# Optimization experiments

Hardware: AMD Instinct MI355X
Metric: run time of the kernel (lower is better)

Reference implementation:

```python
import jax, jax.numpy as jnp
import numpy as np

H, DK, DV = 16, 64, 64

def setup_inputs() -> dict:
    key = jax.random.key(0)
    ks = jax.random.split(key, 5)
    S, E = 2048, 1024
    return {
        "x": jax.random.normal(ks[0], (S, E), jnp.float32),
        "Wq": jax.random.normal(ks[1], (H * DK, E), jnp.float32) * 0.02,
        "Wk": jax.random.normal(ks[2], (H * DK, E), jnp.float32) * 0.02,
        "Wv": jax.random.normal(ks[3], (H * DV, E), jnp.float32) * 0.02,
        "Wo": jax.random.normal(ks[4], (H * DV, H * DV), jnp.float32) * 0.02,
    }

def reference(x, Wq, Wk, Wv, Wo):
    S = x.shape[0]
    # Fused QKV projections (equivalent to per-head Linear with concatenated weights)
    Q = (x @ Wq.T).reshape(S, H, DK).transpose(1, 0, 2)  # [H,S,dk]
    K = (x @ Wk.T).reshape(S, H, DK).transpose(1, 0, 2)  # [H,S,dk]
    V = (x @ Wv.T).reshape(S, H, DV).transpose(1, 0, 2)  # [H,S,dv]
    scale = 1.0 / np.sqrt(DK).astype(np.float32)
    scores = jnp.einsum('hsd,htd->hst', Q, K) * scale    # [H,S,S]
    weights = jax.nn.softmax(scores, axis=-1)
    A = jnp.einsum('hst,htv->hsv', weights, V)           # [H,S,dv]
    A1 = A.transpose(1, 0, 2).reshape(S, H * DV)         # concat heads on last dim
    return A1 @ Wo.T
```

## Files before the change

kernel.cpp:

```cpp
#include <hip/hip_runtime.h>
#include <hip/hip_bf16.h>
#include <stdint.h>

typedef uint16_t u16;
typedef uint32_t u32;
typedef float    f32x4  __attribute__((ext_vector_type(4)));
typedef __bf16   bf16x8 __attribute__((ext_vector_type(8)));
typedef uint16_t u16x8  __attribute__((ext_vector_type(8)));
typedef uint16_t u16x4  __attribute__((ext_vector_type(4)));
typedef uint32_t u32x4  __attribute__((ext_vector_type(4)));

#define HH 16
#define SS 2048
#define EE 1024
#define DD 64

__device__ inline u16 f2bf(float f) {
  uint32_t u = __builtin_bit_cast(uint32_t, f);
  u += 0x7fff + ((u >> 16) & 1);
  return (u16)(u >> 16);
}
__device__ inline float bf2f(u16 b) {
  return __builtin_bit_cast(float, (uint32_t)b << 16);
}

__device__ inline u32 cvtpk(float lo, float hi) {
  u32 r;
  asm("v_cvt_pk_bf16_f32 %0, %1, %2" : "=v"(r) : "v"(lo), "v"(hi));
  return r;
}

__device__ inline void gload_lds16(const void* g, void* l) {
  __builtin_amdgcn_global_load_lds(
      (const __attribute__((address_space(1))) uint32_t*)g,
      (__attribute__((address_space(3))) uint32_t*)l, 16, 0, 0);
}

__global__ __launch_bounds__(256) void convert_kernel(
    const float* __restrict__ x,  const float* __restrict__ wq,
    const float* __restrict__ wk, const float* __restrict__ wv,
    const float* __restrict__ wo,
    u16* __restrict__ xb, u16* __restrict__ wqkvb, u16* __restrict__ wob) {
  const int64_t M1 = 1024 * 1024;
  int64_t e = ((int64_t)blockIdx.x * 256 + threadIdx.x) * 4;
  const float* src; u16* dst; int64_t off;
  if (e < 2 * M1)      { src = x;  dst = xb;           off = e; }
  else if (e < 3 * M1) { src = wq; dst = wqkvb;        off = e - 2 * M1; }
  else if (e < 4 * M1) { src = wk; dst = wqkvb + M1;   off = e - 3 * M1; }
  else if (e < 5 * M1) { src = wv; dst = wqkvb + 2*M1; off = e - 4 * M1; }
  else                 { src = wo; dst = wob;          off = e - 5 * M1; }
  float4 v = *(const float4*)(src + off);
  u16x4 o;
  o[0] = f2bf(v.x); o[1] = f2bf(v.y); o[2] = f2bf(v.z); o[3] = f2bf(v.w);
  *(u16x4*)(dst + off) = o;
}

template <int EPI, int K, int N, int BN>
__global__ __launch_bounds__(256, 4) void gemm_kernel(
    const u16* __restrict__ A, const u16* __restrict__ B,
    u16* __restrict__ q_ws, u16* __restrict__ k_ws, u16* __restrict__ vt_ws,
    float* __restrict__ Cout) {
  constexpr int BM = 64, BK = 64;
  constexpr int NFB = BN / 32;
  constexpr float C2 = 0.18033688f;
  __shared__ __align__(16) u16 As[BM * BK];
  __shared__ __align__(16) u16 Bs[BN * BK];
  const int t = threadIdx.x;
  const int lane = t & 63, w = t >> 6;
  const int wr = w >> 1, wc = w & 1;
  const int fr = lane & 15, fg = lane >> 4;

  const int nwg = gridDim.x * gridDim.y;
  const int bid = blockIdx.y * gridDim.x + blockIdx.x;
  const int swz = (bid & 7) * (nwg >> 3) + (bid >> 3);
  const int m0 = (swz / gridDim.x) * BM, n0 = (swz % gridDim.x) * BN;

  f32x4 acc[2][NFB] = {};

  for (int k0 = 0; k0 < K; k0 += BK) {
#pragma unroll
    for (int it = 0; it < 2; ++it) {
      const int c = t + it * 256, row = c >> 3, sch = (c & 7) ^ (row & 7);
      gload_lds16(A + (int64_t)(m0 + row) * K + k0 + sch * 8,
                  As + (c & ~63) * 8);
    }
#pragma unroll
    for (int it = 0; it < BN * 8 / 256; ++it) {
      const int c = t + it * 256, row = c >> 3, sch = (c & 7) ^ (row & 7);
      gload_lds16(B + (int64_t)(n0 + row) * K + k0 + sch * 8,
                  Bs + (c & ~63) * 8);
    }
    __syncthreads();
    bf16x8 af[2][2], bfr[NFB][2];
#pragma unroll
    for (int mi = 0; mi < 2; ++mi)
#pragma unroll
      for (int kc = 0; kc < 2; ++kc) {
        const int row = wr * 32 + mi * 16 + fr;
        const int cc = (kc * 4 + fg) ^ (row & 7);
        af[mi][kc] = __builtin_bit_cast(bf16x8, *(const u16x8*)&As[row * 64 + cc * 8]);
      }
#pragma unroll
    for (int ni = 0; ni < NFB; ++ni)
#pragma unroll
      for (int kc = 0; kc < 2; ++kc) {
        const int row = wc * (BN / 2) + ni * 16 + fr;
        const int cc = (kc * 4 + fg) ^ (row & 7);
        bfr[ni][kc] = __builtin_bit_cast(bf16x8, *(const u16x8*)&Bs[row * 64 + cc * 8]);
      }
#pragma unroll
    for (int kc = 0; kc < 2; ++kc)
#pragma unroll
      for (int mi = 0; mi < 2; ++mi)
#pragma unroll
        for (int ni = 0; ni < NFB; ++ni)
          acc[mi][ni] = __builtin_amdgcn_mfma_f32_16x16x32_bf16(
              af[mi][kc], bfr[ni][kc], acc[mi][ni], 0, 0, 0);
    __syncthreads();
  }

#pragma unroll
  for (int mi = 0; mi < 2; ++mi)
#pragma unroll
    for (int ni = 0; ni < NFB; ++ni)
#pragma unroll
      for (int r = 0; r < 4; ++r) {
        const int m = m0 + wr * 32 + mi * 16 + fg * 4 + r;
        const int n = n0 + wc * (BN / 2) + ni * 16 + fr;
        const float v = acc[mi][ni][r];
        if constexpr (EPI == 0) {
          const int which = n >> 10, nn = n & 1023, h = nn >> 6, d = nn & 63;
          if (which == 0)
            q_ws[((int64_t)h * SS + m) * DD + d] = f2bf(v * C2);
          else if (which == 1)
            k_ws[((int64_t)h * SS + m) * DD + d] = f2bf(v);
          else
            vt_ws[((int64_t)h * DD + d) * SS + m] = f2bf(v);
        } else {
          Cout[(int64_t)m * N + n] = v;
        }
      }
}

__global__ __launch_bounds__(256, 5) void attn_kernel(
    const u16* __restrict__ q_ws, const u16* __restrict__ k_ws,
    const u16* __restrict__ vt_ws, u16* __restrict__ opart,
    float* __restrict__ lsum) {
  constexpr int NTS = SS / 64 / 2;
  __shared__ __align__(16) u16 lds[16384];
  const int t = threadIdx.x;
  const int lane = t & 63, w = t >> 6;
  const int ql = lane & 15, g = lane >> 4;
  const int h = blockIdx.y, qb = blockIdx.x, sp = blockIdx.z;
  const int kt0 = sp * NTS;
  const int qbase = qb * 64 + w * 16;

  const u16* Qh = q_ws + ((int64_t)h * SS + qbase) * DD;
  const u16* Kh = k_ws + ((int64_t)h * SS + kt0 * 64) * DD;
  const u16* Vh = vt_ws + (int64_t)h * DD * SS + kt0 * 64;

  const int r0 = t >> 3, ch = t & 7, r1 = (t + 256) >> 3;
  const int sch0 = ch ^ (r0 & 7), sch1 = ch ^ (r1 & 7);
  const int64_t ko0 = (int64_t)r0 * DD + sch0 * 8;
  const int64_t ko1 = (int64_t)r1 * DD + sch1 * 8;
  const int64_t vo0 = (int64_t)r0 * SS + sch0 * 8;
  const int64_t vo1 = (int64_t)r1 * SS + sch1 * 8;
  const int dst0 = (t & ~63) * 8, dst1 = dst0 + 2048;

  bf16x8 qf[2];
#pragma unroll
  for (int dd = 0; dd < 2; ++dd)
    qf[dd] = __builtin_bit_cast(
        bf16x8, *(const u16x8*)(Qh + ql * DD + dd * 32 + g * 8));

  u16x8 ov;
#pragma unroll
  for (int j = 0; j < 8; ++j) ov[j] = 0x3F80;
  const bf16x8 onesf = __builtin_bit_cast(bf16x8, ov);

  f32x4 o[4] = {};
  f32x4 o_l = {};

  auto qk = [&](f32x4 (&s)[4], const int kb_) {
    __builtin_amdgcn_s_setprio(1);
#pragma unroll
    for (int kb = 0; kb < 4; ++kb) {
      const int key = kb * 16 + ql;
      f32x4 z = {};
#pragma unroll
      for (int dd = 0; dd < 2; ++dd) {
        bf16x8 kf = __builtin_bit_cast(
            bf16x8,
            *(const u16x8*)&lds[kb_ * 4096 + key * 64 +
                                (((dd * 4 + g) ^ (ql & 7)) * 8)]);
        z = __builtin_amdgcn_mfma_f32_16x16x32_bf16(kf, qf[dd], z, 0, 0, 0);
      }
      s[kb] = z;
    }
    __builtin_amdgcn_s_setprio(0);
  };

  auto smpv = [&](f32x4 (&s)[4], const int vb_) {
#pragma unroll
    for (int kb = 0; kb < 4; ++kb)
#pragma unroll
      for (int r = 0; r < 4; ++r)
        s[kb][r] = exp2f(s[kb][r]);
#pragma unroll
    for (int ks = 0; ks < 2; ++ks) {
      u32 x0 = cvtpk(s[2 * ks][0], s[2 * ks][1]);
      u32 x1 = cvtpk(s[2 * ks][2], s[2 * ks][3]);
      u32 y0 = cvtpk(s[2 * ks + 1][0], s[2 * ks + 1][1]);
      u32 y1 = cvtpk(s[2 * ks + 1][2], s[2 * ks + 1][3]);
      asm("v_permlane32_swap_b32 %0, %1" : "+v"(x0), "+v"(y0));
      asm("v_permlane16_swap_b32 %0, %1" : "+v"(x0), "+v"(y0));
      asm("v_permlane32_swap_b32 %0, %1" : "+v"(x1), "+v"(y1));
      asm("v_permlane16_swap_b32 %0, %1" : "+v"(x1), "+v"(y1));
      u32x4 aw; aw[0] = x0; aw[1] = x1; aw[2] = y0; aw[3] = y1;
      const bf16x8 pa = __builtin_bit_cast(bf16x8, aw);
      __builtin_amdgcn_s_setprio(1);
      o_l = __builtin_amdgcn_mfma_f32_16x16x32_bf16(pa, onesf, o_l, 0, 0, 0);
#pragma unroll
      for (int nb = 0; nb < 4; ++nb) {
        const int dv = nb * 16 + ql;
        bf16x8 vf = __builtin_bit_cast(
            bf16x8,
            *(const u16x8*)&lds[8192 + vb_ * 4096 + dv * 64 +
                                (((ks * 4 + g) ^ (ql & 7)) * 8)]);
        o[nb] = __builtin_amdgcn_mfma_f32_16x16x32_bf16(pa, vf, o[nb], 0, 0, 0);
      }
      __builtin_amdgcn_s_setprio(0);
    }
  };

  gload_lds16(Kh + ko0, lds + dst0);
  gload_lds16(Kh + ko1, lds + dst1);

  f32x4 sA[4], sB[4];
#pragma unroll
  for (int tt = 0; tt < NTS; ++tt) {
    __syncthreads();
    if (tt + 1 < NTS) {
      const u16* Kn = Kh + (int64_t)(tt + 1) * 64 * DD;
      const int kb = ((tt + 1) & 1) * 4096;
      gload_lds16(Kn + ko0, lds + kb + dst0);
      gload_lds16(Kn + ko1, lds + kb + dst1);
    }
    {
      const u16* Vn = Vh + tt * 64;
      const int vb = 8192 + (tt & 1) * 4096;
      gload_lds16(Vn + vo0, lds + vb + dst0);
      gload_lds16(Vn + vo1, lds + vb + dst1);
    }
    if (tt & 1) {
      qk(sB, tt & 1);
      smpv(sA, (tt - 1) & 1);
    } else {
      qk(sA, tt & 1);
      if (tt > 0) smpv(sB, (tt - 1) & 1);
    }
  }
  __syncthreads();
  smpv(sB, (NTS - 1) & 1);

  const int64_t rowbase = ((int64_t)sp * HH + h) * SS;
#pragma unroll
  for (int r = 0; r < 4; ++r) {
    const int q = qbase + g * 4 + r;
#pragma unroll
    for (int nb = 0; nb < 4; ++nb)
      opart[(rowbase + q) * DD + nb * 16 + ql] = f2bf(o[nb][r]);
  }
  if (ql == 0) {
#pragma unroll
    for (int r = 0; r < 4; ++r)
      lsum[rowbase + qbase + g * 4 + r] = o_l[r];
  }
}

__global__ __launch_bounds__(256) void combine_kernel(
    const u16* __restrict__ opart, const float* __restrict__ lsum,
    u16* __restrict__ a_ws) {
  const int rid = blockIdx.x * 4 + (threadIdx.x >> 6);
  const int lane = threadIdx.x & 63;
  const int h = rid >> 11, q = rid & 2047;
  const float inv = 1.0f / (lsum[rid] + lsum[HH * SS + rid]);
  const float o1 = bf2f(opart[(int64_t)rid * DD + lane]);
  const float o2 = bf2f(opart[((int64_t)HH * SS + rid) * DD + lane]);
  a_ws[(int64_t)q * (HH * DD) + h * DD + lane] = f2bf((o1 + o2) * inv);
}

extern "C" void kernel_launch(void* const* d_in, const int* in_sizes, int n_in,
                              void* d_out, int out_size, void* d_ws, size_t ws_size,
                              hipStream_t stream) {
  const float* x  = (const float*)d_in[0];
  const float* wq = (const float*)d_in[1];
  const float* wk = (const float*)d_in[2];
  const float* wv = (const float*)d_in[3];
  const float* wo = (const float*)d_in[4];
  char* ws = (char*)d_ws;
  const int64_t Mi = 1 << 20;
  u16* xb    = (u16*)(ws + 0 * Mi);
  u16* wqkv  = (u16*)(ws + 4 * Mi);
  u16* wob   = (u16*)(ws + 10 * Mi);
  u16* q_ws  = (u16*)(ws + 12 * Mi);
  u16* k_ws  = (u16*)(ws + 16 * Mi);
  u16* vt    = (u16*)(ws + 20 * Mi);
  u16*   opart = (u16*)(ws + 0 * Mi);
  float* lsv   = (float*)(ws + 8 * Mi);
  u16* a_ws  = (u16*)(ws + 12 * Mi);
  float* out = (float*)d_out;

  convert_kernel<<<6144, 256, 0, stream>>>(x, wq, wk, wv, wo, xb, wqkv, wob);

  gemm_kernel<0, 1024, 3072, 128><<<dim3(3072 / 128, 2048 / 64), 256, 0, stream>>>(
      xb, wqkv, q_ws, k_ws, vt, nullptr);

  attn_kernel<<<dim3(SS / 64, HH, 2), 256, 0, stream>>>(
      q_ws, k_ws, vt, opart, lsv);

  combine_kernel<<<HH * SS / 4, 256, 0, stream>>>(opart, lsv, a_ws);

  gemm_kernel<1, 1024, 1024, 64><<<dim3(1024 / 64, 2048 / 64), 256, 0, stream>>>(
      a_ws, wob, nullptr, nullptr, nullptr, out);
}
```

Baseline: 82.83 us.

## Process 32 query rows per wave in attention to reuse K/V LDS fragments

Each wave now handles two 16-row query tiles instead of one, so a block covers 128 queries and the grid is halved. Every K and V fragment read from LDS feeds two MFMAs, halving the LDS reads and global K/V loads per unit of work. The cost is roughly double the accumulator and score registers per wave, so launch bounds drop from 5 to 2 and occupancy falls. With fewer blocks there is less parallelism to hide latency.

```diff
diff --git a/kernel.cpp b/kernel.cpp
--- a/kernel.cpp
+++ b/kernel.cpp
@@ -142,7 +142,7 @@
       }
 }
 
-__global__ __launch_bounds__(256, 5) void attn_kernel(
+__global__ __launch_bounds__(256, 2) void attn_kernel(
     const u16* __restrict__ q_ws, const u16* __restrict__ k_ws,
     const u16* __restrict__ vt_ws, u16* __restrict__ opart,
     float* __restrict__ lsum) {
@@ -153,7 +153,7 @@
   const int ql = lane & 15, g = lane >> 4;
   const int h = blockIdx.y, qb = blockIdx.x, sp = blockIdx.z;
   const int kt0 = sp * NTS;
-  const int qbase = qb * 64 + w * 16;
+  const int qbase = qb * 128 + w * 32;
 
   const u16* Qh = q_ws + ((int64_t)h * SS + qbase) * DD;
   const u16* Kh = k_ws + ((int64_t)h * SS + kt0 * 64) * DD;
@@ -167,59 +167,76 @@
   const int64_t vo1 = (int64_t)r1 * SS + sch1 * 8;
   const int dst0 = (t & ~63) * 8, dst1 = dst0 + 2048;
 
-  bf16x8 qf[2];
-#pragma unroll
-  for (int dd = 0; dd < 2; ++dd)
-    qf[dd] = __builtin_bit_cast(
+  bf16x8 qfl[2], qfh[2];
+#pragma unroll
+  for (int dd = 0; dd < 2; ++dd) {
+    qfl[dd] = __builtin_bit_cast(
         bf16x8, *(const u16x8*)(Qh + ql * DD + dd * 32 + g * 8));
+    qfh[dd] = __builtin_bit_cast(
+        bf16x8, *(const u16x8*)(Qh + (ql + 16) * DD + dd * 32 + g * 8));
+  }
 
   u16x8 ov;
 #pragma unroll
   for (int j = 0; j < 8; ++j) ov[j] = 0x3F80;
   const bf16x8 onesf = __builtin_bit_cast(bf16x8, ov);
 
-  f32x4 o[4] = {};
-  f32x4 o_l = {};
-
-  auto qk = [&](f32x4 (&s)[4], const int kb_) {
+  f32x4 ol[4] = {}, oh[4] = {};
+  f32x4 o_ll = {}, o_lh = {};
+
+  auto qk = [&](f32x4 (&sl)[4], f32x4 (&sh)[4], const int kb_) {
     __builtin_amdgcn_s_setprio(1);
 #pragma unroll
     for (int kb = 0; kb < 4; ++kb) {
       const int key = kb * 16 + ql;
-      f32x4 z = {};
+      f32x4 zl = {}, zh = {};
 #pragma unroll
       for (int dd = 0; dd < 2; ++dd) {
         bf16x8 kf = __builtin_bit_cast(
             bf16x8,
             *(const u16x8*)&lds[kb_ * 4096 + key * 64 +
                                 (((dd * 4 + g) ^ (ql & 7)) * 8)]);
-        z = __builtin_amdgcn_mfma_f32_16x16x32_bf16(kf, qf[dd], z, 0, 0, 0);
-      }
-      s[kb] = z;
+        zl = __builtin_amdgcn_mfma_f32_16x16x32_bf16(kf, qfl[dd], zl, 0, 0, 0);
+        zh = __builtin_amdgcn_mfma_f32_16x16x32_bf16(kf, qfh[dd], zh, 0, 0, 0);
+      }
+      sl[kb] = zl; sh[kb] = zh;
     }
     __builtin_amdgcn_s_setprio(0);
   };
 
-  auto smpv = [&](f32x4 (&s)[4], const int vb_) {
+  auto smpv = [&](f32x4 (&sl)[4], f32x4 (&sh)[4], const int vb_) {
 #pragma unroll
     for (int kb = 0; kb < 4; ++kb)
 #pragma unroll
-      for (int r = 0; r < 4; ++r)
-        s[kb][r] = exp2f(s[kb][r]);
+      for (int r = 0; r < 4; ++r) {
+        sl[kb][r] = exp2f(sl[kb][r]);
+        sh[kb][r] = exp2f(sh[kb][r]);
+      }
 #pragma unroll
     for (int ks = 0; ks < 2; ++ks) {
-      u32 x0 = cvtpk(s[2 * ks][0], s[2 * ks][1]);
-      u32 x1 = cvtpk(s[2 * ks][2], s[2 * ks][3]);
-      u32 y0 = cvtpk(s[2 * ks + 1][0], s[2 * ks + 1][1]);
-      u32 y1 = cvtpk(s[2 * ks + 1][2], s[2 * ks + 1][3]);
-      asm("v_permlane32_swap_b32 %0, %1" : "+v"(x0), "+v"(y0));
-      asm("v_permlane16_swap_b32 %0, %1" : "+v"(x0), "+v"(y0));
-      asm("v_permlane32_swap_b32 %0, %1" : "+v"(x1), "+v"(y1));
-      asm("v_permlane16_swap_b32 %0, %1" : "+v"(x1), "+v"(y1));
-      u32x4 aw; aw[0] = x0; aw[1] = x1; aw[2] = y0; aw[3] = y1;
-      const bf16x8 pa = __builtin_bit_cast(bf16x8, aw);
+      u32 xl0 = cvtpk(sl[2 * ks][0], sl[2 * ks][1]);
+      u32 xl1 = cvtpk(sl[2 * ks][2], sl[2 * ks][3]);
+      u32 yl0 = cvtpk(sl[2 * ks + 1][0], sl[2 * ks + 1][1]);
+      u32 yl1 = cvtpk(sl[2 * ks + 1][2], sl[2 * ks + 1][3]);
+      asm("v_permlane32_swap_b32 %0, %1" : "+v"(xl0), "+v"(yl0));
+      asm("v_permlane16_swap_b32 %0, %1" : "+v"(xl0), "+v"(yl0));
+      asm("v_permlane32_swap_b32 %0, %1" : "+v"(xl1), "+v"(yl1));
+      asm("v_permlane16_swap_b32 %0, %1" : "+v"(xl1), "+v"(yl1));
+      u32x4 awl; awl[0] = xl0; awl[1] = xl1; awl[2] = yl0; awl[3] = yl1;
+      const bf16x8 pal = __builtin_bit_cast(bf16x8, awl);
+      u32 xh0 = cvtpk(sh[2 * ks][0], sh[2 * ks][1]);
+      u32 xh1 = cvtpk(sh[2 * ks][2], sh[2 * ks][3]);
+      u32 yh0 = cvtpk(sh[2 * ks + 1][0], sh[2 * ks + 1][1]);
+      u32 yh1 = cvtpk(sh[2 * ks + 1][2], sh[2 * ks + 1][3]);
+      asm("v_permlane32_swap_b32 %0, %1" : "+v"(xh0), "+v"(yh0));
+      asm("v_permlane16_swap_b32 %0, %1" : "+v"(xh0), "+v"(yh0));
+      asm("v_permlane32_swap_b32 %0, %1" : "+v"(xh1), "+v"(yh1));
+      asm("v_permlane16_swap_b32 %0, %1" : "+v"(xh1), "+v"(yh1));
+      u32x4 awh; awh[0] = xh0; awh[1] = xh1; awh[2] = yh0; awh[3] = yh1;
+      const bf16x8 pah = __builtin_bit_cast(bf16x8, awh);
       __builtin_amdgcn_s_setprio(1);
-      o_l = __builtin_amdgcn_mfma_f32_16x16x32_bf16(pa, onesf, o_l, 0, 0, 0);
+      o_ll = __builtin_amdgcn_mfma_f32_16x16x32_bf16(pal, onesf, o_ll, 0, 0, 0);
+      o_lh = __builtin_amdgcn_mfma_f32_16x16x32_bf16(pah, onesf, o_lh, 0, 0, 0);
 #pragma unroll
       for (int nb = 0; nb < 4; ++nb) {
         const int dv = nb * 16 + ql;
@@ -227,7 +244,8 @@
             bf16x8,
             *(const u16x8*)&lds[8192 + vb_ * 4096 + dv * 64 +
                                 (((ks * 4 + g) ^ (ql & 7)) * 8)]);
-        o[nb] = __builtin_amdgcn_mfma_f32_16x16x32_bf16(pa, vf, o[nb], 0, 0, 0);
+        ol[nb] = __builtin_amdgcn_mfma_f32_16x16x32_bf16(pal, vf, ol[nb], 0, 0, 0);
+        oh[nb] = __builtin_amdgcn_mfma_f32_16x16x32_bf16(pah, vf, oh[nb], 0, 0, 0);
       }
       __builtin_amdgcn_s_setprio(0);
     }
@@ -236,7 +254,7 @@
   gload_lds16(Kh + ko0, lds + dst0);
   gload_lds16(Kh + ko1, lds + dst1);
 
-  f32x4 sA[4], sB[4];
+  f32x4 sAl[4], sAh[4], sBl[4], sBh[4];
 #pragma unroll
   for (int tt = 0; tt < NTS; ++tt) {
     __syncthreads();
@@ -253,28 +271,32 @@
       gload_lds16(Vn + vo1, lds + vb + dst1);
     }
     if (tt & 1) {
-      qk(sB, tt & 1);
-      smpv(sA, (tt - 1) & 1);
+      qk(sBl, sBh, tt & 1);
+      smpv(sAl, sAh, (tt - 1) & 1);
     } else {
-      qk(sA, tt & 1);
-      if (tt > 0) smpv(sB, (tt - 1) & 1);
+      qk(sAl, sAh, tt & 1);
+      if (tt > 0) smpv(sBl, sBh, (tt - 1) & 1);
     }
   }
   __syncthreads();
-  smpv(sB, (NTS - 1) & 1);
+  smpv(sBl, sBh, (NTS - 1) & 1);
 
   const int64_t rowbase = ((int64_t)sp * HH + h) * SS;
 #pragma unroll
   for (int r = 0; r < 4; ++r) {
     const int q = qbase + g * 4 + r;
 #pragma unroll
-    for (int nb = 0; nb < 4; ++nb)
-      opart[(rowbase + q) * DD + nb * 16 + ql] = f2bf(o[nb][r]);
+    for (int nb = 0; nb < 4; ++nb) {
+      opart[(rowbase + q) * DD + nb * 16 + ql] = f2bf(ol[nb][r]);
+      opart[(rowbase + q + 16) * DD + nb * 16 + ql] = f2bf(oh[nb][r]);
+    }
   }
   if (ql == 0) {
 #pragma unroll
-    for (int r = 0; r < 4; ++r)
-      lsum[rowbase + qbase + g * 4 + r] = o_l[r];
+    for (int r = 0; r < 4; ++r) {
+      lsum[rowbase + qbase + g * 4 + r] = o_ll[r];
+      lsum[rowbase + qbase + 16 + g * 4 + r] = o_lh[r];
+    }
   }
 }
 
@@ -316,7 +338,7 @@
   gemm_kernel<0, 1024, 3072, 128><<<dim3(3072 / 128, 2048 / 64), 256, 0, stream>>>(
       xb, wqkv, q_ws, k_ws, vt, nullptr);
 
-  attn_kernel<<<dim3(SS / 64, HH, 2), 256, 0, stream>>>(
+  attn_kernel<<<dim3(SS / 128, HH, 2), 256, 0, stream>>>(
       q_ws, k_ws, vt, opart, lsv);
 
   combine_kernel<<<HH * SS / 4, 256, 0, stream>>>(opart, lsv, a_ws);
```

Measured after the change: 80.77 us (median of 2 runs). 2.5% less time.
